# Kernel optimization log

Hardware: AMD Instinct MI355X
Metric: run time of the kernel (lower is better)

The kernel has to match this reference:

```python
import jax, jax.numpy as jnp
import numpy as np

B, S, H = 2, 2048, 1024
I = 1024          # moe_intermediate_size
E = 8             # n_routed_experts
K = 2             # num_experts_per_tok
SCALE = 1.0       # routed_scaling_factor


def setup_inputs() -> dict:
    key = jax.random.key(0)
    ks = jax.random.split(key, 8)
    sd = 1.0 / np.sqrt(H)
    si = 1.0 / np.sqrt(I)
    return {
        "hidden_states": jax.random.normal(ks[0], (B, S, H), jnp.float32),
        "router_w": jax.random.uniform(ks[1], (E, H), jnp.float32, -sd, sd),
        # shared expert (n_shared_experts = 1); weights stored [in, out]
        "shared_gate": jax.random.uniform(ks[2], (H, I), jnp.float32, -sd, sd),
        "shared_up": jax.random.uniform(ks[3], (H, I), jnp.float32, -sd, sd),
        "shared_down": jax.random.uniform(ks[4], (I, H), jnp.float32, -si, si),
        # routed experts, stacked [E, in, out]
        "experts_gate": jax.random.uniform(ks[5], (E, H, I), jnp.float32, -sd, sd),
        "experts_up": jax.random.uniform(ks[6], (E, H, I), jnp.float32, -sd, sd),
        "experts_down": jax.random.uniform(ks[7], (E, I, H), jnp.float32, -si, si),
    }


def reference(hidden_states, router_w, shared_gate, shared_up, shared_down,
              experts_gate, experts_up, experts_down):
    residual = hidden_states
    x = hidden_states.reshape(-1, H)                      # [T, H], T = B*S

    # shared expert (SwiGLU-ish: sigmoid(gate) * up)
    sg = x @ shared_gate
    su = x @ shared_up
    shared_out = (jax.nn.sigmoid(sg) * su) @ shared_down  # [T, H]

    # router: softmax over experts, greedy top-k
    logits = x @ router_w.T                               # [T, E]
    scores = jax.nn.softmax(logits.astype(jnp.float32), axis=-1)
    topk_w, topk_idx = jax.lax.top_k(scores, K)           # [T, K]
    topk_w = topk_w * SCALE

    # dense compute of ALL experts on all tokens (faithful to reference)
    g = jnp.einsum('th,ehi->tei', x, experts_gate)        # [T, E, I]
    u = jnp.einsum('th,ehi->tei', x, experts_up)
    hid = jax.nn.sigmoid(g) * u
    expert_outputs = jnp.einsum('tei,eih->teh', hid, experts_down)  # [T, E, H]

    # gather top-k expert outputs and combine
    selected = jnp.take_along_axis(expert_outputs, topk_idx[:, :, None], axis=1)  # [T, K, H]
    routed_out = (selected * topk_w[:, :, None]).sum(axis=1)                      # [T, H]

    out = residual + (shared_out + routed_out).reshape(B, S, H)
    return out
```

## Files before the change

kernel.cpp:

```cpp
#include <hip/hip_runtime.h>
#include <hip/hip_bf16.h>

#define T_TOK 4096
#define HDIM 1024
#define IDIM 1024
#define EDIM 8
#define HID_SHARED_BASE 8320

typedef __attribute__((ext_vector_type(8))) short bf16x8;
typedef __attribute__((ext_vector_type(4))) float f32x4;

static __device__ __forceinline__ unsigned short f2bf(float f) {
  union { float f; unsigned int u; } v; v.f = f;
  unsigned int u = v.u;
  unsigned int r = u + 0x7FFFu + ((u >> 16) & 1u);
  return (unsigned short)(r >> 16);
}
static __device__ __forceinline__ float bf2f(unsigned short s) {
  union { unsigned int u; float f; } v; v.u = ((unsigned int)s) << 16;
  return v.f;
}

#define GLD16(g, l) __builtin_amdgcn_global_load_lds( \
    (const __attribute__((address_space(1))) void*)(g), \
    (__attribute__((address_space(3))) void*)(l), 16, 0, 0)

__global__ __launch_bounds__(256) void convert_x(const float4* __restrict__ x4,
                                                 ushort4* __restrict__ xb4,
                                                 float4* __restrict__ out4,
                                                 int* __restrict__ cnt, int initOut) {
  int i = blockIdx.x * 256 + threadIdx.x;
  if (blockIdx.x == 0 && threadIdx.x < 16) cnt[threadIdx.x] = 0;
  float4 v = x4[i];
  if (initOut) out4[i] = v;
  ushort4 o;
  o.x = f2bf(v.x); o.y = f2bf(v.y); o.z = f2bf(v.z); o.w = f2bf(v.w);
  xb4[i] = o;
}

struct SrcPtrs { const float* p[6]; };

__global__ __launch_bounds__(256) void transpose_all(SrcPtrs S,
                                                     unsigned short* __restrict__ dstBase) {
  const int z = blockIdx.z;
  const float* src; int dz;
  if (z == 0)      { src = S.p[0];                              dz = 8;  }
  else if (z == 1) { src = S.p[1];                              dz = 17; }
  else if (z == 2) { src = S.p[2];                              dz = 26; }
  else if (z < 11) { src = S.p[3] + (size_t)(z - 3)  * 1048576; dz = z - 3; }
  else if (z < 19) { src = S.p[4] + (size_t)(z - 11) * 1048576; dz = 9 + (z - 11); }
  else             { src = S.p[5] + (size_t)(z - 19) * 1048576; dz = 18 + (z - 19); }
  unsigned short* dst = dstBase + (size_t)dz * 1048576;

  const int tid = threadIdx.x;
  const int rid = tid & 7;
  const int cid = tid >> 3;
  const int r = blockIdx.y * 64 + rid * 8;
  const int c = blockIdx.x * 128 + cid * 4;

  float4 v[8];
#pragma unroll
  for (int i = 0; i < 8; i++)
    v[i] = *(const float4*)&src[(size_t)(r + i) * 1024 + c];

#pragma unroll
  for (int j = 0; j < 4; j++) {
    unsigned short o[8];
    o[0] = f2bf(v[0][j]); o[1] = f2bf(v[1][j]);
    o[2] = f2bf(v[2][j]); o[3] = f2bf(v[3][j]);
    o[4] = f2bf(v[4][j]); o[5] = f2bf(v[5][j]);
    o[6] = f2bf(v[6][j]); o[7] = f2bf(v[7][j]);
    *(bf16x8*)&dst[(size_t)(c + j) * 1024 + r] = *(const bf16x8*)o;
  }
}

__global__ __launch_bounds__(256) void router2(
    const float* __restrict__ x, const float* __restrict__ rw,
    int* __restrict__ cnt, int* __restrict__ list, float* __restrict__ wgt) {
  __shared__ float rwT[1024 * 8];
  const int tid = threadIdx.x;
#pragma unroll
  for (int c = 0; c < 4; c++) {
    const int h = c * 256 + tid;
    float v[8];
#pragma unroll
    for (int e = 0; e < EDIM; e++) v[e] = rw[e * 1024 + h];
    *(float4*)&rwT[h * 8]     = make_float4(v[0], v[1], v[2], v[3]);
    *(float4*)&rwT[h * 8 + 4] = make_float4(v[4], v[5], v[6], v[7]);
  }
  __syncthreads();

  const int tt = tid >> 4;
  const int pp = tid & 15;
  const int t = blockIdx.x * 16 + tt;
  const float* xr = x + (size_t)t * HDIM;

  float a[EDIM];
#pragma unroll
  for (int e = 0; e < EDIM; e++) a[e] = 0.f;

#pragma unroll 8
  for (int i = 0; i < 64; i++) {
    const int h = pp + 16 * i;
    const float xs = xr[h];
    const float4 r0 = *(const float4*)&rwT[h * 8];
    const float4 r1 = *(const float4*)&rwT[h * 8 + 4];
    a[0] += xs * r0.x; a[1] += xs * r0.y; a[2] += xs * r0.z; a[3] += xs * r0.w;
    a[4] += xs * r1.x; a[5] += xs * r1.y; a[6] += xs * r1.z; a[7] += xs * r1.w;
  }
#pragma unroll
  for (int s = 1; s < 16; s <<= 1) {
#pragma unroll
    for (int e = 0; e < EDIM; e++) a[e] += __shfl_xor(a[e], s, 16);
  }
  if (pp == 0) {
    float m = a[0];
#pragma unroll
    for (int e = 1; e < EDIM; e++) m = fmaxf(m, a[e]);
    float p[EDIM]; float s = 0.f;
#pragma unroll
    for (int e = 0; e < EDIM; e++) { p[e] = expf(a[e] - m); s += p[e]; }
    float inv = 1.f / s;
    int e1 = 0; float b1 = p[0];
#pragma unroll
    for (int e = 1; e < EDIM; e++) if (p[e] > b1) { b1 = p[e]; e1 = e; }
    int e2 = -1; float b2 = -1.f;
#pragma unroll
    for (int e = 0; e < EDIM; e++) if (e != e1 && p[e] > b2) { b2 = p[e]; e2 = e; }
    int pos1 = atomicAdd(&cnt[e1], 1);
    list[e1 * T_TOK + pos1] = (t << 1);      wgt[e1 * T_TOK + pos1] = b1 * inv;
    int pos2 = atomicAdd(&cnt[e2], 1);
    list[e2 * T_TOK + pos2] = (t << 1) | 1;  wgt[e2 * T_TOK + pos2] = b2 * inv;
  }
}

__global__ __launch_bounds__(256) void gateup_f(
    const unsigned short* __restrict__ xb,
    const unsigned short* __restrict__ gateT,
    const unsigned short* __restrict__ upT,
    unsigned short* __restrict__ hid,
    const int* __restrict__ cnt, const int* __restrict__ list) {
  __shared__ unsigned short Al[3][128 * 32];
  __shared__ unsigned short Bg[3][64 * 32];
  __shared__ unsigned short Bu[3][64 * 32];

  const int tid = threadIdx.x;
  const int lane = tid & 63;
  const int w = tid >> 6;
  const int wm = w >> 1, wn = w & 1;
  const int z = blockIdx.z;
  const int m0 = blockIdx.y * 128;
  const int n0 = blockIdx.x * 64;

  int count, hidbase;
  if (z < EDIM) {
    count = cnt[z];
    if (m0 >= count) return;
    int off = 0;
#pragma unroll
    for (int i = 0; i < EDIM; i++) off += (i < z) ? cnt[i] : 0;
    hidbase = off;
  } else {
    count = T_TOK;
    hidbase = HID_SHARED_BASE;
  }
  const unsigned short* wg = gateT + (size_t)z * HDIM * IDIM;
  const unsigned short* wu = upT   + (size_t)z * HDIM * IDIM;

  const unsigned short* gA[2];
#pragma unroll
  for (int j = 0; j < 2; j++) {
    const int s = w * 128 + j * 64 + lane;
    const int row = s >> 2;
    const int g = (s & 3) ^ ((row + (row >> 2)) & 3);
    int tok;
    if (z < EDIM) {
      int p = m0 + row; if (p >= count) p = count - 1;
      tok = list[z * T_TOK + p] >> 1;
    } else tok = m0 + row;
    gA[j] = xb + (size_t)tok * HDIM + g * 8;
  }
  const int sB = w * 64 + lane;
  const int rowB = sB >> 2;
  const int gB = (sB & 3) ^ ((rowB + (rowB >> 2)) & 3);
  const unsigned short* gGp = wg + (size_t)(n0 + rowB) * HDIM + gB * 8;
  const unsigned short* gUp = wu + (size_t)(n0 + rowB) * HDIM + gB * 8;

  f32x4 accg[4][2], accu[4][2];
  const f32x4 z4 = {0.f, 0.f, 0.f, 0.f};
#pragma unroll
  for (int i = 0; i < 4; i++)
#pragma unroll
    for (int j = 0; j < 2; j++) { accg[i][j] = z4; accu[i][j] = z4; }

  const int q = lane >> 4;
  const int r16 = lane & 15;
  const int ch = (q ^ ((r16 + (r16 >> 2)) & 3)) * 8;

  auto stage = [&](int k0, int b) {
    GLD16(gA[0] + k0, &Al[b][(w * 128) * 8]);
    GLD16(gA[1] + k0, &Al[b][(w * 128 + 64) * 8]);
    GLD16(gGp + k0, &Bg[b][(w * 64) * 8]);
    GLD16(gUp + k0, &Bu[b][(w * 64) * 8]);
  };
  auto compute = [&](int b) {
    bf16x8 af[4], bg2[2], bu2[2];
#pragma unroll
    for (int i = 0; i < 4; i++)
      af[i] = *(const bf16x8*)&Al[b][(wm * 64 + i * 16 + r16) * 32 + ch];
#pragma unroll
    for (int j = 0; j < 2; j++) {
      bg2[j] = *(const bf16x8*)&Bg[b][(wn * 32 + j * 16 + r16) * 32 + ch];
      bu2[j] = *(const bf16x8*)&Bu[b][(wn * 32 + j * 16 + r16) * 32 + ch];
    }
#pragma unroll
    for (int i = 0; i < 4; i++)
#pragma unroll
      for (int j = 0; j < 2; j++) {
        accg[i][j] = __builtin_amdgcn_mfma_f32_16x16x32_bf16(af[i], bg2[j], accg[i][j], 0, 0, 0);
        accu[i][j] = __builtin_amdgcn_mfma_f32_16x16x32_bf16(af[i], bu2[j], accu[i][j], 0, 0, 0);
      }
  };

  stage(0, 0);
  stage(32, 1);
#pragma unroll 1
  for (int p = 0; p < 32; p++) {
    if (p < 30) {
      asm volatile("s_waitcnt vmcnt(4)" ::: "memory");
    } else {
      asm volatile("s_waitcnt vmcnt(0)" ::: "memory");
    }
    __builtin_amdgcn_s_barrier();
    if (p + 2 < 32) stage((p + 2) * 32, (p + 2) % 3);
    compute(p % 3);
  }

#pragma unroll
  for (int i = 0; i < 4; i++) {
#pragma unroll
    for (int j = 0; j < 2; j++) {
      const int col = n0 + wn * 32 + j * 16 + r16;
#pragma unroll
      for (int r = 0; r < 4; r++) {
        int pos = m0 + wm * 64 + i * 16 + q * 4 + r;
        if (pos < count) {
          float g = accg[i][j][r], u = accu[i][j][r];
          float h = u / (1.f + __expf(-g));
          hid[(size_t)(hidbase + pos) * IDIM + col] = f2bf(h);
        }
      }
    }
  }
}

__global__ __launch_bounds__(256) void down_f(
    const unsigned short* __restrict__ hid,
    const unsigned short* __restrict__ downT,
    float* __restrict__ out, unsigned short* __restrict__ R, int useR,
    const int* __restrict__ cnt, const int* __restrict__ list,
    const float* __restrict__ wgt) {
  __shared__ unsigned short Al[3][128 * 32];
  __shared__ unsigned short Bl[3][128 * 32];

  const int tid = threadIdx.x;
  const int lane = tid & 63;
  const int w = tid >> 6;
  const int wm = w >> 1, wn = w & 1;
  const int z = blockIdx.z;
  const int m0 = blockIdx.y * 128;
  const int n0 = blockIdx.x * 128;

  int count, abase;
  if (z < EDIM) {
    count = cnt[z];
    if (m0 >= count) return;
    int off = 0;
#pragma unroll
    for (int i = 0; i < EDIM; i++) off += (i < z) ? cnt[i] : 0;
    abase = off;
  } else {
    count = T_TOK;
    abase = HID_SHARED_BASE;
  }
  const unsigned short* wd = downT + (size_t)z * IDIM * HDIM;

  const unsigned short *gA[2], *gBp[2];
#pragma unroll
  for (int j = 0; j < 2; j++) {
    const int s = w * 128 + j * 64 + lane;
    const int row = s >> 2;
    const int g = (s & 3) ^ ((row + (row >> 2)) & 3);
    gA[j]  = hid + (size_t)(abase + m0 + row) * IDIM + g * 8;
    gBp[j] = wd + (size_t)(n0 + row) * IDIM + g * 8;
  }

  f32x4 acc[4][4];
  const f32x4 z4 = {0.f, 0.f, 0.f, 0.f};
#pragma unroll
  for (int i = 0; i < 4; i++)
#pragma unroll
    for (int j = 0; j < 4; j++) acc[i][j] = z4;

  const int q = lane >> 4;
  const int r16 = lane & 15;
  const int ch = (q ^ ((r16 + (r16 >> 2)) & 3)) * 8;

  auto stage = [&](int k0, int b) {
    GLD16(gA[0] + k0,  &Al[b][(w * 128) * 8]);
    GLD16(gA[1] + k0,  &Al[b][(w * 128 + 64) * 8]);
    GLD16(gBp[0] + k0, &Bl[b][(w * 128) * 8]);
    GLD16(gBp[1] + k0, &Bl[b][(w * 128 + 64) * 8]);
  };
  auto compute = [&](int b) {
    bf16x8 af[4], bf4[4];
#pragma unroll
    for (int i = 0; i < 4; i++)
      af[i] = *(const bf16x8*)&Al[b][(wm * 64 + i * 16 + r16) * 32 + ch];
#pragma unroll
    for (int j = 0; j < 4; j++)
      bf4[j] = *(const bf16x8*)&Bl[b][(wn * 64 + j * 16 + r16) * 32 + ch];
#pragma unroll
    for (int i = 0; i < 4; i++)
#pragma unroll
      for (int j = 0; j < 4; j++)
        acc[i][j] = __builtin_amdgcn_mfma_f32_16x16x32_bf16(af[i], bf4[j], acc[i][j], 0, 0, 0);
  };

  stage(0, 0);
  stage(32, 1);
#pragma unroll 1
  for (int p = 0; p < 32; p++) {
    if (p < 30) {
      asm volatile("s_waitcnt vmcnt(4)" ::: "memory");
    } else {
      asm volatile("s_waitcnt vmcnt(0)" ::: "memory");
    }
    __builtin_amdgcn_s_barrier();
    if (p + 2 < 32) stage((p + 2) * 32, (p + 2) % 3);
    compute(p % 3);
  }

#pragma unroll
  for (int i = 0; i < 4; i++) {
    int toks[4]; int slot[4]; float ws4[4];
#pragma unroll
    for (int r = 0; r < 4; r++) {
      int pos = m0 + wm * 64 + i * 16 + q * 4 + r;
      if (z < EDIM) {
        bool ok = pos < count;
        int v = ok ? list[z * T_TOK + pos] : -2;
        toks[r] = v >> 1; slot[r] = v & 1;
        ws4[r] = ok ? wgt[z * T_TOK + pos] : 0.f;
      } else {
        toks[r] = pos; slot[r] = 2; ws4[r] = 1.f;
      }
    }
#pragma unroll
    for (int j = 0; j < 4; j++) {
      const int col = n0 + wn * 64 + j * 16 + r16;
#pragma unroll
      for (int r = 0; r < 4; r++) {
        if (toks[r] >= 0) {
          float v = ws4[r] * acc[i][j][r];
          if (useR) {
            R[((size_t)toks[r] * 3 + slot[r]) * HDIM + col] = f2bf(v);
          } else {
            atomicAdd(&out[(size_t)toks[r] * HDIM + col], v);
          }
        }
      }
    }
  }
}

__global__ __launch_bounds__(256) void combine_k(const float4* __restrict__ x4,
                                                 const unsigned short* __restrict__ R,
                                                 float4* __restrict__ out4) {
  const int i8 = blockIdx.x * 256 + threadIdx.x;
  const int t = i8 >> 7;
  const int c8 = (i8 & 127) * 8;
  const unsigned short* r0 = R + ((size_t)t * 3) * 1024 + c8;
  float s[8];
#pragma unroll
  for (int k = 0; k < 8; k++) s[k] = 0.f;
#pragma unroll
  for (int sl = 0; sl < 3; sl++) {
    bf16x8 v = *(const bf16x8*)(r0 + sl * 1024);
#pragma unroll
    for (int k = 0; k < 8; k++) s[k] += bf2f(((const unsigned short*)&v)[k]);
  }
  float4 a = x4[i8 * 2], b = x4[i8 * 2 + 1];
  a.x += s[0]; a.y += s[1]; a.z += s[2]; a.w += s[3];
  b.x += s[4]; b.y += s[5]; b.z += s[6]; b.w += s[7];
  out4[i8 * 2] = a;
  out4[i8 * 2 + 1] = b;
}

extern "C" void kernel_launch(void* const* d_in, const int* in_sizes, int n_in,
                              void* d_out, int out_size, void* d_ws, size_t ws_size,
                              hipStream_t stream) {
  const float* x  = (const float*)d_in[0];
  const float* rw = (const float*)d_in[1];
  const float* sg = (const float*)d_in[2];
  const float* su = (const float*)d_in[3];
  const float* sd = (const float*)d_in[4];
  const float* eg = (const float*)d_in[5];
  const float* eu = (const float*)d_in[6];
  const float* ed = (const float*)d_in[7];
  float* out = (float*)d_out;

  char* ws = (char*)d_ws;
  unsigned short* xb  = (unsigned short*)ws;
  unsigned short* hid = xb + (size_t)T_TOK * HDIM;
  int*   cnt  = (int*)(hid + (size_t)(HID_SHARED_BASE + T_TOK) * IDIM);
  int*   list = cnt + 16;
  float* wgt  = (float*)(list + EDIM * T_TOK);
  unsigned short* wT    = (unsigned short*)(wgt + EDIM * T_TOK);
  unsigned short* gateT = wT;
  unsigned short* upT   = wT + (size_t)9 * 1048576;
  unsigned short* downT = wT + (size_t)18 * 1048576;
  unsigned short* R = wT + (size_t)27 * 1048576;
  size_t need = ((char*)(R + (size_t)T_TOK * 3 * HDIM)) - ws;
  const int useR = (ws_size >= need) ? 1 : 0;

  convert_x<<<(T_TOK * HDIM) / 1024, 256, 0, stream>>>(
      (const float4*)x, (ushort4*)xb, (float4*)out, cnt, useR ? 0 : 1);
  router2<<<T_TOK / 16, 256, 0, stream>>>(x, rw, cnt, list, wgt);

  SrcPtrs S; S.p[0] = sg; S.p[1] = su; S.p[2] = sd; S.p[3] = eg; S.p[4] = eu; S.p[5] = ed;
  transpose_all<<<dim3(8, 16, 27), 256, 0, stream>>>(S, wT);

  gateup_f<<<dim3(IDIM / 64, 32, 9), 256, 0, stream>>>(xb, gateT, upT, hid, cnt, list);
  down_f<<<dim3(HDIM / 128, 32, 9), 256, 0, stream>>>(hid, downT, out, R, useR,
                                                      cnt, list, wgt);
  if (useR) {
    combine_k<<<(T_TOK * HDIM / 8) / 256, 256, 0, stream>>>(
        (const float4*)x, R, (float4*)out);
  }
}
```

Measured before the change: 377.0 us.

## Rewrite expert GEMMs with 256x256 tiles, 8 waves and ping-pong LDS pipeline

Replaces the gate/up and down grouped GEMM kernels with 512-thread blocks using 256-row tiles and a 64-wide K step. The schedule is double buffered and interleaves LDS reads, async global-to-LDS loads and MFMA quadrants, with s_setprio around the MFMA groups. Gate and up columns are interleaved into one B tile so each block produces both activations together. The larger tiles raise data reuse per load and cut pipeline overhead, but they waste more work on padding for experts with few tokens and increase register and LDS pressure.

```diff
diff --git a/kernel.cpp b/kernel.cpp
--- a/kernel.cpp
+++ b/kernel.cpp
@@ -134,23 +134,24 @@
   }
 }
 
-__global__ __launch_bounds__(256) void gateup_f(
+
+__global__ __launch_bounds__(512, 2) void gateup8(
     const unsigned short* __restrict__ xb,
     const unsigned short* __restrict__ gateT,
     const unsigned short* __restrict__ upT,
     unsigned short* __restrict__ hid,
     const int* __restrict__ cnt, const int* __restrict__ list) {
-  __shared__ unsigned short Al[3][128 * 32];
-  __shared__ unsigned short Bg[3][64 * 32];
-  __shared__ unsigned short Bu[3][64 * 32];
+  __shared__ __align__(16) unsigned short As[2][256 * 64];
+  __shared__ __align__(16) unsigned short Bs[2][256 * 64];
 
   const int tid = threadIdx.x;
   const int lane = tid & 63;
   const int w = tid >> 6;
-  const int wm = w >> 1, wn = w & 1;
+  const int wm = w >> 2;
+  const int wn = w & 3;
   const int z = blockIdx.z;
-  const int m0 = blockIdx.y * 128;
-  const int n0 = blockIdx.x * 64;
+  const int m0 = blockIdx.y * 256;
+  const int n0 = blockIdx.x * 128;
 
   int count, hidbase;
   if (z < EDIM) {
@@ -164,112 +165,161 @@
     count = T_TOK;
     hidbase = HID_SHARED_BASE;
   }
-  const unsigned short* wg = gateT + (size_t)z * HDIM * IDIM;
-  const unsigned short* wu = upT   + (size_t)z * HDIM * IDIM;
-
-  const unsigned short* gA[2];
-#pragma unroll
-  for (int j = 0; j < 2; j++) {
-    const int s = w * 128 + j * 64 + lane;
-    const int row = s >> 2;
-    const int g = (s & 3) ^ ((row + (row >> 2)) & 3);
-    int tok;
-    if (z < EDIM) {
-      int p = m0 + row; if (p >= count) p = count - 1;
-      tok = list[z * T_TOK + p] >> 1;
-    } else tok = m0 + row;
-    gA[j] = xb + (size_t)tok * HDIM + g * 8;
-  }
-  const int sB = w * 64 + lane;
-  const int rowB = sB >> 2;
-  const int gB = (sB & 3) ^ ((rowB + (rowB >> 2)) & 3);
-  const unsigned short* gGp = wg + (size_t)(n0 + rowB) * HDIM + gB * 8;
-  const unsigned short* gUp = wu + (size_t)(n0 + rowB) * HDIM + gB * 8;
-
-  f32x4 accg[4][2], accu[4][2];
-  const f32x4 z4 = {0.f, 0.f, 0.f, 0.f};
-#pragma unroll
-  for (int i = 0; i < 4; i++)
-#pragma unroll
-    for (int j = 0; j < 2; j++) { accg[i][j] = z4; accu[i][j] = z4; }
+
+  const int l3 = lane >> 3;
+  const unsigned g8 = (unsigned)(((lane & 7) ^ l3) * 8);
+
+  unsigned aOff[2][2], bOff[2][2];
+#pragma unroll
+  for (int h = 0; h < 2; h++) {
+#pragma unroll
+    for (int r = 0; r < 2; r++) {
+      const int rowA = r * 128 + h * 64 + w * 8 + l3;
+      int tok;
+      if (z < EDIM) {
+        int p = m0 + rowA; if (p >= count) p = count - 1;
+        tok = list[z * T_TOK + p] >> 1;
+      } else tok = m0 + rowA;
+      aOff[h][r] = (unsigned)tok * 1024u + g8;
+
+      const int rowB = (w >> 1) * 64 + h * 32 + ((w & 1) * 2 + r) * 8 + l3;
+      const int grp = rowB >> 5, ud = (rowB >> 4) & 1, cc = rowB & 15;
+      const unsigned icol = (unsigned)(n0 + grp * 16 + cc);
+      bOff[h][r] = (unsigned)ud * 9437184u + icol * 1024u + g8;
+    }
+  }
+  const unsigned short* aBase = xb;
+  const unsigned short* bBase = gateT + (size_t)z * (HDIM * IDIM);
+
+  auto stageA = [&](int buf, int kt, int h) {
+#pragma unroll
+    for (int r = 0; r < 2; r++)
+      GLD16(aBase + aOff[h][r] + kt * 64,
+            &As[buf][(r * 128 + h * 64 + w * 8) * 64]);
+  };
+  auto stageB = [&](int buf, int kt, int h) {
+#pragma unroll
+    for (int r = 0; r < 2; r++)
+      GLD16(bBase + bOff[h][r] + kt * 64,
+            &Bs[buf][((w >> 1) * 64 + h * 32 + ((w & 1) * 2 + r) * 8) * 64]);
+  };
 
   const int q = lane >> 4;
   const int r16 = lane & 15;
-  const int ch = (q ^ ((r16 + (r16 >> 2)) & 3)) * 8;
-
-  auto stage = [&](int k0, int b) {
-    GLD16(gA[0] + k0, &Al[b][(w * 128) * 8]);
-    GLD16(gA[1] + k0, &Al[b][(w * 128 + 64) * 8]);
-    GLD16(gGp + k0, &Bg[b][(w * 64) * 8]);
-    GLD16(gUp + k0, &Bu[b][(w * 64) * 8]);
-  };
-  auto compute = [&](int b) {
-    bf16x8 af[4], bg2[2], bu2[2];
+  const int rsw = r16 & 7;
+
+  bf16x8 a0[8], a1[8], b0[4], b1[4];
+  auto readA = [&](int buf, int mh, bf16x8 (&dst)[8]) {
 #pragma unroll
     for (int i = 0; i < 4; i++)
-      af[i] = *(const bf16x8*)&Al[b][(wm * 64 + i * 16 + r16) * 32 + ch];
-#pragma unroll
-    for (int j = 0; j < 2; j++) {
-      bg2[j] = *(const bf16x8*)&Bg[b][(wn * 32 + j * 16 + r16) * 32 + ch];
-      bu2[j] = *(const bf16x8*)&Bu[b][(wn * 32 + j * 16 + r16) * 32 + ch];
-    }
+#pragma unroll
+      for (int kk = 0; kk < 2; kk++)
+        dst[i * 2 + kk] = *(const bf16x8*)&As[buf][
+            (wm * 128 + mh * 64 + i * 16 + r16) * 64 + (((kk * 4 + q) ^ rsw) * 8)];
+  };
+  auto readB = [&](int buf, int nh, bf16x8 (&dst)[4]) {
+#pragma unroll
+    for (int j = 0; j < 2; j++)
+#pragma unroll
+      for (int kk = 0; kk < 2; kk++)
+        dst[j * 2 + kk] = *(const bf16x8*)&Bs[buf][
+            (wn * 64 + nh * 32 + j * 16 + r16) * 64 + (((kk * 4 + q) ^ rsw) * 8)];
+  };
+
+  f32x4 acc[8][4];
+  const f32x4 z4 = {0.f, 0.f, 0.f, 0.f};
+#pragma unroll
+  for (int i = 0; i < 8; i++)
+#pragma unroll
+    for (int j = 0; j < 4; j++) acc[i][j] = z4;
+
+  auto quad = [&](const bf16x8 (&A)[8], const bf16x8 (&B)[4], int mh, int nh) {
 #pragma unroll
     for (int i = 0; i < 4; i++)
 #pragma unroll
-      for (int j = 0; j < 2; j++) {
-        accg[i][j] = __builtin_amdgcn_mfma_f32_16x16x32_bf16(af[i], bg2[j], accg[i][j], 0, 0, 0);
-        accu[i][j] = __builtin_amdgcn_mfma_f32_16x16x32_bf16(af[i], bu2[j], accu[i][j], 0, 0, 0);
-      }
-  };
-
-  stage(0, 0);
-  stage(32, 1);
+      for (int j = 0; j < 2; j++)
+#pragma unroll
+        for (int kk = 0; kk < 2; kk++)
+          acc[mh * 4 + i][nh * 2 + j] = __builtin_amdgcn_mfma_f32_16x16x32_bf16(
+              A[i * 2 + kk], B[j * 2 + kk], acc[mh * 4 + i][nh * 2 + j], 0, 0, 0);
+  };
+
+  const int NT = 16;
+  stageA(0, 0, 0); stageA(0, 0, 1); stageB(0, 0, 0); stageB(0, 0, 1);
+  stageA(1, 1, 0); stageA(1, 1, 1); stageB(1, 1, 0);
+  asm volatile("s_waitcnt vmcnt(6)" ::: "memory");
+  __builtin_amdgcn_s_barrier();
+
 #pragma unroll 1
-  for (int p = 0; p < 32; p++) {
-    if (p < 30) {
-      asm volatile("s_waitcnt vmcnt(4)" ::: "memory");
-    } else {
-      asm volatile("s_waitcnt vmcnt(0)" ::: "memory");
-    }
-    __builtin_amdgcn_s_barrier();
-    if (p + 2 < 32) stage((p + 2) * 32, (p + 2) % 3);
-    compute(p % 3);
-  }
-
-#pragma unroll
-  for (int i = 0; i < 4; i++) {
-#pragma unroll
-    for (int j = 0; j < 2; j++) {
-      const int col = n0 + wn * 32 + j * 16 + r16;
+  for (int kt = 0; kt < NT; kt++) {
+    const int buf = kt & 1;
+    readA(buf, 0, a0);
+    readB(buf, 0, b0);
+    if (kt + 1 < NT) stageB(buf ^ 1, kt + 1, 1);
+    asm volatile("s_waitcnt lgkmcnt(0)" ::: "memory");
+    __builtin_amdgcn_s_setprio(1);
+    quad(a0, b0, 0, 0);
+    __builtin_amdgcn_s_setprio(0);
+    __builtin_amdgcn_s_barrier();
+    readA(buf, 1, a1);
+    if (kt + 2 < NT) stageA(buf, kt + 2, 0);
+    asm volatile("s_waitcnt lgkmcnt(0)" ::: "memory");
+    __builtin_amdgcn_s_setprio(1);
+    quad(a1, b0, 1, 0);
+    __builtin_amdgcn_s_setprio(0);
+    __builtin_amdgcn_s_barrier();
+    readB(buf, 1, b1);
+    if (kt + 2 < NT) stageA(buf, kt + 2, 1);
+    asm volatile("s_waitcnt lgkmcnt(0)" ::: "memory");
+    __builtin_amdgcn_s_setprio(1);
+    quad(a1, b1, 1, 1);
+    __builtin_amdgcn_s_setprio(0);
+    __builtin_amdgcn_s_barrier();
+    if (kt + 2 < NT) stageB(buf, kt + 2, 0);
+    __builtin_amdgcn_s_setprio(1);
+    quad(a0, b1, 0, 1);
+    __builtin_amdgcn_s_setprio(0);
+    if (kt + 2 < NT) { asm volatile("s_waitcnt vmcnt(6)" ::: "memory"); }
+    else             { asm volatile("s_waitcnt vmcnt(0)" ::: "memory"); }
+    __builtin_amdgcn_s_barrier();
+  }
+
+#pragma unroll
+  for (int i = 0; i < 8; i++) {
+#pragma unroll
+    for (int nh = 0; nh < 2; nh++) {
+      const int icol = n0 + (wn * 2 + nh) * 16 + r16;
+      f32x4 g4 = acc[i][nh * 2 + 0];
+      f32x4 u4 = acc[i][nh * 2 + 1];
 #pragma unroll
       for (int r = 0; r < 4; r++) {
-        int pos = m0 + wm * 64 + i * 16 + q * 4 + r;
+        const int pos = m0 + wm * 128 + i * 16 + q * 4 + r;
         if (pos < count) {
-          float g = accg[i][j][r], u = accu[i][j][r];
-          float h = u / (1.f + __expf(-g));
-          hid[(size_t)(hidbase + pos) * IDIM + col] = f2bf(h);
+          float h = u4[r] / (1.f + __expf(-g4[r]));
+          hid[(size_t)(hidbase + pos) * IDIM + icol] = f2bf(h);
         }
       }
     }
   }
 }
 
-__global__ __launch_bounds__(256) void down_f(
+__global__ __launch_bounds__(512, 2) void down8(
     const unsigned short* __restrict__ hid,
     const unsigned short* __restrict__ downT,
     float* __restrict__ out, unsigned short* __restrict__ R, int useR,
     const int* __restrict__ cnt, const int* __restrict__ list,
     const float* __restrict__ wgt) {
-  __shared__ unsigned short Al[3][128 * 32];
-  __shared__ unsigned short Bl[3][128 * 32];
+  __shared__ __align__(16) unsigned short As[2][256 * 64];
+  __shared__ __align__(16) unsigned short Bs[2][256 * 64];
 
   const int tid = threadIdx.x;
   const int lane = tid & 63;
   const int w = tid >> 6;
-  const int wm = w >> 1, wn = w & 1;
+  const int wm = w >> 2;
+  const int wn = w & 3;
   const int z = blockIdx.z;
-  const int m0 = blockIdx.y * 128;
-  const int n0 = blockIdx.x * 128;
+  const int m0 = blockIdx.y * 256;
+  const int n0 = blockIdx.x * 256;
 
   int count, abase;
   if (z < EDIM) {
@@ -283,70 +333,126 @@
     count = T_TOK;
     abase = HID_SHARED_BASE;
   }
-  const unsigned short* wd = downT + (size_t)z * IDIM * HDIM;
-
-  const unsigned short *gA[2], *gBp[2];
-#pragma unroll
-  for (int j = 0; j < 2; j++) {
-    const int s = w * 128 + j * 64 + lane;
-    const int row = s >> 2;
-    const int g = (s & 3) ^ ((row + (row >> 2)) & 3);
-    gA[j]  = hid + (size_t)(abase + m0 + row) * IDIM + g * 8;
-    gBp[j] = wd + (size_t)(n0 + row) * IDIM + g * 8;
-  }
-
-  f32x4 acc[4][4];
-  const f32x4 z4 = {0.f, 0.f, 0.f, 0.f};
-#pragma unroll
-  for (int i = 0; i < 4; i++)
-#pragma unroll
-    for (int j = 0; j < 4; j++) acc[i][j] = z4;
+
+  const int l3 = lane >> 3;
+  const unsigned g8 = (unsigned)(((lane & 7) ^ l3) * 8);
+
+  unsigned aOff[2][2], bOff[2][2];
+#pragma unroll
+  for (int h = 0; h < 2; h++) {
+#pragma unroll
+    for (int r = 0; r < 2; r++) {
+      const int rowA = r * 128 + h * 64 + w * 8 + l3;
+      aOff[h][r] = (unsigned)(abase + m0 + rowA) * 1024u + g8;
+      const int rowB = (w >> 1) * 64 + h * 32 + ((w & 1) * 2 + r) * 8 + l3;
+      bOff[h][r] = (unsigned)(n0 + rowB) * 1024u + g8;
+    }
+  }
+  const unsigned short* aBase = hid;
+  const unsigned short* bBase = downT + (size_t)z * (IDIM * HDIM);
+
+  auto stageA = [&](int buf, int kt, int h) {
+#pragma unroll
+    for (int r = 0; r < 2; r++)
+      GLD16(aBase + aOff[h][r] + kt * 64,
+            &As[buf][(r * 128 + h * 64 + w * 8) * 64]);
+  };
+  auto stageB = [&](int buf, int kt, int h) {
+#pragma unroll
+    for (int r = 0; r < 2; r++)
+      GLD16(bBase + bOff[h][r] + kt * 64,
+            &Bs[buf][((w >> 1) * 64 + h * 32 + ((w & 1) * 2 + r) * 8) * 64]);
+  };
 
   const int q = lane >> 4;
   const int r16 = lane & 15;
-  const int ch = (q ^ ((r16 + (r16 >> 2)) & 3)) * 8;
-
-  auto stage = [&](int k0, int b) {
-    GLD16(gA[0] + k0,  &Al[b][(w * 128) * 8]);
-    GLD16(gA[1] + k0,  &Al[b][(w * 128 + 64) * 8]);
-    GLD16(gBp[0] + k0, &Bl[b][(w * 128) * 8]);
-    GLD16(gBp[1] + k0, &Bl[b][(w * 128 + 64) * 8]);
-  };
-  auto compute = [&](int b) {
-    bf16x8 af[4], bf4[4];
+  const int rsw = r16 & 7;
+
+  bf16x8 a0[8], a1[8], b0[4], b1[4];
+  auto readA = [&](int buf, int mh, bf16x8 (&dst)[8]) {
 #pragma unroll
     for (int i = 0; i < 4; i++)
-      af[i] = *(const bf16x8*)&Al[b][(wm * 64 + i * 16 + r16) * 32 + ch];
-#pragma unroll
-    for (int j = 0; j < 4; j++)
-      bf4[j] = *(const bf16x8*)&Bl[b][(wn * 64 + j * 16 + r16) * 32 + ch];
+#pragma unroll
+      for (int kk = 0; kk < 2; kk++)
+        dst[i * 2 + kk] = *(const bf16x8*)&As[buf][
+            (wm * 128 + mh * 64 + i * 16 + r16) * 64 + (((kk * 4 + q) ^ rsw) * 8)];
+  };
+  auto readB = [&](int buf, int nh, bf16x8 (&dst)[4]) {
+#pragma unroll
+    for (int j = 0; j < 2; j++)
+#pragma unroll
+      for (int kk = 0; kk < 2; kk++)
+        dst[j * 2 + kk] = *(const bf16x8*)&Bs[buf][
+            (wn * 64 + nh * 32 + j * 16 + r16) * 64 + (((kk * 4 + q) ^ rsw) * 8)];
+  };
+
+  f32x4 acc[8][4];
+  const f32x4 z4 = {0.f, 0.f, 0.f, 0.f};
+#pragma unroll
+  for (int i = 0; i < 8; i++)
+#pragma unroll
+    for (int j = 0; j < 4; j++) acc[i][j] = z4;
+
+  auto quad = [&](const bf16x8 (&A)[8], const bf16x8 (&B)[4], int mh, int nh) {
 #pragma unroll
     for (int i = 0; i < 4; i++)
 #pragma unroll
-      for (int j = 0; j < 4; j++)
-        acc[i][j] = __builtin_amdgcn_mfma_f32_16x16x32_bf16(af[i], bf4[j], acc[i][j], 0, 0, 0);
-  };
-
-  stage(0, 0);
-  stage(32, 1);
+      for (int j = 0; j < 2; j++)
+#pragma unroll
+        for (int kk = 0; kk < 2; kk++)
+          acc[mh * 4 + i][nh * 2 + j] = __builtin_amdgcn_mfma_f32_16x16x32_bf16(
+              A[i * 2 + kk], B[j * 2 + kk], acc[mh * 4 + i][nh * 2 + j], 0, 0, 0);
+  };
+
+  const int NT = 16;
+  stageA(0, 0, 0); stageA(0, 0, 1); stageB(0, 0, 0); stageB(0, 0, 1);
+  stageA(1, 1, 0); stageA(1, 1, 1); stageB(1, 1, 0);
+  asm volatile("s_waitcnt vmcnt(6)" ::: "memory");
+  __builtin_amdgcn_s_barrier();
+
 #pragma unroll 1
-  for (int p = 0; p < 32; p++) {
-    if (p < 30) {
-      asm volatile("s_waitcnt vmcnt(4)" ::: "memory");
-    } else {
-      asm volatile("s_waitcnt vmcnt(0)" ::: "memory");
-    }
-    __builtin_amdgcn_s_barrier();
-    if (p + 2 < 32) stage((p + 2) * 32, (p + 2) % 3);
-    compute(p % 3);
-  }
-
-#pragma unroll
-  for (int i = 0; i < 4; i++) {
+  for (int kt = 0; kt < NT; kt++) {
+    const int buf = kt & 1;
+    readA(buf, 0, a0);
+    readB(buf, 0, b0);
+    if (kt + 1 < NT) stageB(buf ^ 1, kt + 1, 1);
+    asm volatile("s_waitcnt lgkmcnt(0)" ::: "memory");
+    __builtin_amdgcn_s_setprio(1);
+    quad(a0, b0, 0, 0);
+    __builtin_amdgcn_s_setprio(0);
+    __builtin_amdgcn_s_barrier();
+
+    readA(buf, 1, a1);
+    if (kt + 2 < NT) stageA(buf, kt + 2, 0);
+    asm volatile("s_waitcnt lgkmcnt(0)" ::: "memory");
+    __builtin_amdgcn_s_setprio(1);
+    quad(a1, b0, 1, 0);
+    __builtin_amdgcn_s_setprio(0);
+    __builtin_amdgcn_s_barrier();
+
+    readB(buf, 1, b1);
+    if (kt + 2 < NT) stageA(buf, kt + 2, 1);
+    asm volatile("s_waitcnt lgkmcnt(0)" ::: "memory");
+    __builtin_amdgcn_s_setprio(1);
+    quad(a1, b1, 1, 1);
+    __builtin_amdgcn_s_setprio(0);
+    __builtin_amdgcn_s_barrier();
+
+    if (kt + 2 < NT) stageB(buf, kt + 2, 0);
+    __builtin_amdgcn_s_setprio(1);
+    quad(a0, b1, 0, 1);
+    __builtin_amdgcn_s_setprio(0);
+    if (kt + 2 < NT) { asm volatile("s_waitcnt vmcnt(6)" ::: "memory"); }
+    else             { asm volatile("s_waitcnt vmcnt(0)" ::: "memory"); }
+    __builtin_amdgcn_s_barrier();
+  }
+
+#pragma unroll
+  for (int i = 0; i < 8; i++) {
     int toks[4]; int slot[4]; float ws4[4];
 #pragma unroll
     for (int r = 0; r < 4; r++) {
-      int pos = m0 + wm * 64 + i * 16 + q * 4 + r;
+      const int pos = m0 + wm * 128 + i * 16 + q * 4 + r;
       if (z < EDIM) {
         bool ok = pos < count;
         int v = ok ? list[z * T_TOK + pos] : -2;
@@ -358,7 +464,7 @@
     }
 #pragma unroll
     for (int j = 0; j < 4; j++) {
-      const int col = n0 + wn * 64 + j * 16 + r16;
+      const int col = n0 + wn * 64 + (j >> 1) * 32 + (j & 1) * 16 + r16;
 #pragma unroll
       for (int r = 0; r < 4; r++) {
         if (toks[r] >= 0) {
@@ -431,9 +537,9 @@
   SrcPtrs S; S.p[0] = sg; S.p[1] = su; S.p[2] = sd; S.p[3] = eg; S.p[4] = eu; S.p[5] = ed;
   transpose_all<<<dim3(8, 16, 27), 256, 0, stream>>>(S, wT);
 
-  gateup_f<<<dim3(IDIM / 64, 32, 9), 256, 0, stream>>>(xb, gateT, upT, hid, cnt, list);
-  down_f<<<dim3(HDIM / 128, 32, 9), 256, 0, stream>>>(hid, downT, out, R, useR,
-                                                      cnt, list, wgt);
+  gateup8<<<dim3(IDIM / 128, 16, 9), 512, 0, stream>>>(xb, gateT, upT, hid, cnt, list);
+  down8<<<dim3(HDIM / 256, 16, 9), 512, 0, stream>>>(hid, downT, out, R, useR,
+                                                     cnt, list, wgt);
   if (useR) {
     combine_k<<<(T_TOK * HDIM / 8) / 256, 256, 0, stream>>>(
         (const float4*)x, R, (float4*)out);
```

New measurement: 384.9 us. 1.02x slower.
